# Kernel optimization log

Measured on AMD Instinct MI355X. Metric: run time of the kernel, lower is better.

## Reference

```python
import jax, jax.numpy as jnp
import numpy as np

HIDDEN = 3072
INTER = 8192
B, S = 4, 2048


def setup_inputs() -> dict:
    key = jax.random.key(0)
    k1, k2, k3, k4, k5 = jax.random.split(key, 5)
    hidden_states = jax.random.normal(k1, (B, S, HIDDEN), dtype=jnp.float32)
    # int8-valued quantized weights (stored as int32), per-output-channel scales
    gate_up_w_q = jax.random.randint(k2, (2 * INTER, HIDDEN), -128, 128, dtype=jnp.int32)
    gate_up_scale = jax.random.uniform(k3, (2 * INTER,), dtype=jnp.float32) * 0.01
    down_w_q = jax.random.randint(k4, (HIDDEN, INTER), -128, 128, dtype=jnp.int32)
    down_scale = jax.random.uniform(k5, (HIDDEN,), dtype=jnp.float32) * 0.01
    return {
        "hidden_states": hidden_states,
        "gate_up_w_q": gate_up_w_q,
        "gate_up_scale": gate_up_scale,
        "down_w_q": down_w_q,
        "down_scale": down_scale,
    }


def reference(hidden_states, gate_up_w_q, gate_up_scale, down_w_q, down_scale):
    # Inline dequant: W = W_q * scale (per output channel)
    w_gu = gate_up_w_q.astype(jnp.float32) * gate_up_scale[:, None]   # [2I, H]
    up_states = jnp.einsum("bsh,oh->bso", hidden_states, w_gu)        # [B, S, 2I]
    gate, up = jnp.split(up_states, 2, axis=-1)                       # each [B, S, I]
    h = up * jax.nn.silu(gate)                                        # SwiGLU
    w_d = down_w_q.astype(jnp.float32) * down_scale[:, None]          # [H, I]
    return jnp.einsum("bsi,hi->bsh", h, w_d)                          # [B, S, H]
```

## Files before the change

kernel.cpp:

```cpp
#include <hip/hip_runtime.h>
#include <hip/hip_bf16.h>

#define HIDDEN 3072
#define INTER  8192
#define NTOK   8192

typedef __attribute__((ext_vector_type(8))) short bf16x8;
typedef __attribute__((ext_vector_type(4))) float f32x4;

__device__ __forceinline__ void gload_lds16(const void* g, void* l) {
  __builtin_amdgcn_global_load_lds(
      (const __attribute__((address_space(1))) void*)g,
      (__attribute__((address_space(3))) void*)l, 16, 0, 0);
}

__device__ __forceinline__ unsigned short f2bf(float f) {
  unsigned int u = __builtin_bit_cast(unsigned int, f);
  u += 0x7fffu + ((u >> 16) & 1u);
  return (unsigned short)(u >> 16);
}


__global__ void cvt_f32_bf16(const float* __restrict__ in,
                             unsigned short* __restrict__ out, int n4) {
  int i = blockIdx.x * blockDim.x + threadIdx.x;
  if (i >= n4) return;
  float4 v = reinterpret_cast<const float4*>(in)[i];
  ushort4 o;
  o.x = f2bf(v.x); o.y = f2bf(v.y); o.z = f2bf(v.z); o.w = f2bf(v.w);
  reinterpret_cast<ushort4*>(out)[i] = o;
}

__global__ void cvt_i32_bf16(const int* __restrict__ in,
                             unsigned short* __restrict__ out, int n4) {
  int i = blockIdx.x * blockDim.x + threadIdx.x;
  if (i >= n4) return;
  int4 v = reinterpret_cast<const int4*>(in)[i];
  ushort4 o;
  o.x = f2bf((float)v.x); o.y = f2bf((float)v.y);
  o.z = f2bf((float)v.z); o.w = f2bf((float)v.w);
  reinterpret_cast<ushort4*>(out)[i] = o;
}

__global__ void cvt_wgu_perm(const int* __restrict__ in,
                             unsigned short* __restrict__ out) {
  int i4 = blockIdx.x * blockDim.x + threadIdx.x;
  const int RW = HIDDEN / 4;
  if (i4 >= 2 * INTER * RW) return;
  int rowp = i4 / RW;
  int col4 = i4 - rowp * RW;
  int c = ((rowp >> 5) << 4) + (rowp & 15);
  int u = (rowp >> 4) & 1;
  int srow = u * INTER + c;
  int4 v = reinterpret_cast<const int4*>(in)[(size_t)srow * RW + col4];
  ushort4 o;
  o.x = f2bf((float)v.x); o.y = f2bf((float)v.y);
  o.z = f2bf((float)v.z); o.w = f2bf((float)v.w);
  reinterpret_cast<ushort4*>(out)[i4] = o;
}


template<int K, int N>
__global__ __launch_bounds__(512, 2) void gemm8p(
    const unsigned short* __restrict__ A,
    const unsigned short* __restrict__ B,
    const float* __restrict__ scale,
    unsigned short* __restrict__ H)
{
  constexpr int NT = K / 64;
  __shared__ __align__(16) unsigned short lds[2][2][2][256 * 32];

  const int nbn = N / 256;
  const int nwg = (NTOK / 256) * nbn;
  int bid = blockIdx.x;
  int wg = (bid & 7) * (nwg >> 3) + (bid >> 3);
  const int bm = (wg / nbn) * 256;
  const int bn = (wg % nbn) * 256;

  const int tid  = threadIdx.x;
  const int lane = tid & 63;
  const int wid  = tid >> 6;
  const int wr = wid >> 2;
  const int wc = wid & 3;

  const int srow0 = tid >> 2;
  const int srow1 = 128 + (tid >> 2);
  const int scb   = tid & 3;

  const unsigned short* Ab = A + (size_t)bm * K;
  const unsigned short* Bb = B + (size_t)bn * K;

  auto stage = [&](const unsigned short* Gb, int op, int tt, int kh) {
    if (tt >= NT) return;
    int p = tt & 1;
    int kc = tt * 64 + kh * 32;
    unsigned short* lbase = &lds[p][op][kh][0];
    gload_lds16(Gb + (size_t)srow0 * K + kc + ((scb ^ ((srow0 >> 1) & 3)) * 8),
                lbase + (size_t)tid * 8);
    gload_lds16(Gb + (size_t)srow1 * K + kc + ((scb ^ ((srow1 >> 1) & 3)) * 8),
                lbase + (size_t)(512 + tid) * 8);
  };

  auto readA = [&](int p, int kh, int m) -> bf16x8 {
    int row = wr * 128 + m * 16 + (lane & 15);
    int cb = (lane >> 4) ^ ((row >> 1) & 3);
    return *(const bf16x8*)&lds[p][0][kh][row * 32 + cb * 8];
  };
  auto readB = [&](int p, int kh, int n) -> bf16x8 {
    int row = wc * 64 + n * 16 + (lane & 15);
    int cb = (lane >> 4) ^ ((row >> 1) & 3);
    return *(const bf16x8*)&lds[p][1][kh][row * 32 + cb * 8];
  };

  f32x4 acc[8][4] = {};
  bf16x8 aP[4], aQ[4], bP[4], bQ[4];

  stage(Ab, 0, 0, 0);
  stage(Bb, 1, 0, 0);
  stage(Ab, 0, 0, 1);
  stage(Bb, 1, 0, 1);
  asm volatile("s_waitcnt vmcnt(4)" ::: "memory");
  __builtin_amdgcn_s_barrier();
#pragma unroll
  for (int m = 0; m < 4; ++m) aP[m] = readA(0, 0, m);
#pragma unroll
  for (int n = 0; n < 4; ++n) bP[n] = readB(0, 0, n);

  for (int t = 0; t < NT; ++t) {
    const int pr = t & 1;

#pragma unroll
    for (int m = 0; m < 4; ++m) aQ[m] = readA(pr, 0, m + 4);
    stage(Ab, 0, t + 1, 0);
    __builtin_amdgcn_s_setprio(1);
#pragma unroll
    for (int m = 0; m < 4; ++m)
#pragma unroll
      for (int n = 0; n < 4; ++n)
        acc[m][n] = __builtin_amdgcn_mfma_f32_16x16x32_bf16(aP[m], bP[n], acc[m][n], 0, 0, 0);
    __builtin_amdgcn_s_setprio(0);

    if (t + 1 < NT) {
      asm volatile("s_waitcnt vmcnt(2)" ::: "memory");
    } else {
      asm volatile("s_waitcnt vmcnt(0)" ::: "memory");
    }
    __builtin_amdgcn_s_barrier();
#pragma unroll
    for (int m = 0; m < 4; ++m) aP[m] = readA(pr, 1, m);
#pragma unroll
    for (int n = 0; n < 4; ++n) bQ[n] = readB(pr, 1, n);
    stage(Bb, 1, t + 1, 0);
    __builtin_amdgcn_s_setprio(1);
#pragma unroll
    for (int m = 0; m < 4; ++m)
#pragma unroll
      for (int n = 0; n < 4; ++n)
        acc[m + 4][n] = __builtin_amdgcn_mfma_f32_16x16x32_bf16(aQ[m], bP[n], acc[m + 4][n], 0, 0, 0);
    __builtin_amdgcn_s_setprio(0);

#pragma unroll
    for (int m = 0; m < 4; ++m) aQ[m] = readA(pr, 1, m + 4);
    stage(Ab, 0, t + 1, 1);
    __builtin_amdgcn_s_setprio(1);
#pragma unroll
    for (int m = 0; m < 4; ++m)
#pragma unroll
      for (int n = 0; n < 4; ++n)
        acc[m][n] = __builtin_amdgcn_mfma_f32_16x16x32_bf16(aP[m], bQ[n], acc[m][n], 0, 0, 0);
    __builtin_amdgcn_s_setprio(0);

    asm volatile("s_waitcnt vmcnt(2)" ::: "memory");
    __builtin_amdgcn_s_barrier();
    if (t + 1 < NT) {
#pragma unroll
      for (int m = 0; m < 4; ++m) aP[m] = readA(pr ^ 1, 0, m);
#pragma unroll
      for (int n = 0; n < 4; ++n) bP[n] = readB(pr ^ 1, 0, n);
    }
    stage(Bb, 1, t + 1, 1);
    __builtin_amdgcn_s_setprio(1);
#pragma unroll
    for (int m = 0; m < 4; ++m)
#pragma unroll
      for (int n = 0; n < 4; ++n)
        acc[m + 4][n] = __builtin_amdgcn_mfma_f32_16x16x32_bf16(aQ[m], bQ[n], acc[m + 4][n], 0, 0, 0);
    __builtin_amdgcn_s_setprio(0);
  }

  const int crow0 = (lane >> 4) * 4;
  const int ccol  = lane & 15;
  const int hbase = (bn >> 1) + wc * 32;
#pragma unroll
  for (int np = 0; np < 2; ++np) {
    int hcol = hbase + np * 16 + ccol;
    float sg = scale[hcol];
    float su = scale[INTER + hcol];
#pragma unroll
    for (int m = 0; m < 8; ++m) {
#pragma unroll
      for (int j = 0; j < 4; ++j) {
        int row = bm + wr * 128 + m * 16 + crow0 + j;
        float g = acc[m][2 * np + 0][j] * sg;
        float u = acc[m][2 * np + 1][j] * su;
        float s = g / (1.0f + __expf(-g));
        H[(size_t)row * INTER + hcol] = f2bf(u * s);
      }
    }
  }
}


__global__ __launch_bounds__(512, 2) void gemm2k(
    const unsigned short* __restrict__ A,
    const unsigned short* __restrict__ B,
    const float* __restrict__ scale,
    float* __restrict__ O)
{
  constexpr int K = INTER;
  constexpr int NT = K / 64;
  __shared__ __align__(16) unsigned short ldsA[2][2][128 * 32];
  __shared__ __align__(16) unsigned short ldsB[2][2][256 * 32];

  const int nbn = HIDDEN / 256;
  const int nwg = (NTOK / 128) * nbn;
  int bid = blockIdx.x;
  int wg = (bid & 7) * (nwg >> 3) + (bid >> 3);
  const int bm = (wg / nbn) * 128;
  const int bn = (wg % nbn) * 256;

  const int tid  = threadIdx.x;
  const int lane = tid & 63;
  const int wid  = tid >> 6;
  const int wr = wid >> 2;
  const int wc = wid & 3;

  const int srow0 = tid >> 2;
  const int srow1 = 128 + (tid >> 2);
  const int scb   = tid & 3;

  const unsigned short* Ab = A + (size_t)bm * K;
  const unsigned short* Bb = B + (size_t)bn * K;

  auto stageA = [&](int tt, int kh) {
    if (tt >= NT) return;
    int p = tt & 1;
    int kc = tt * 64 + kh * 32;
    gload_lds16(Ab + (size_t)srow0 * K + kc + ((scb ^ ((srow0 >> 1) & 3)) * 8),
                &ldsA[p][kh][0] + (size_t)tid * 8);
  };
  auto stageB = [&](int tt, int kh) {
    if (tt >= NT) return;
    int p = tt & 1;
    int kc = tt * 64 + kh * 32;
    unsigned short* lbase = &ldsB[p][kh][0];
    gload_lds16(Bb + (size_t)srow0 * K + kc + ((scb ^ ((srow0 >> 1) & 3)) * 8),
                lbase + (size_t)tid * 8);
    gload_lds16(Bb + (size_t)srow1 * K + kc + ((scb ^ ((srow1 >> 1) & 3)) * 8),
                lbase + (size_t)(512 + tid) * 8);
  };

  auto readA = [&](int p, int kh, int m) -> bf16x8 {
    int row = wr * 64 + m * 16 + (lane & 15);
    int cb = (lane >> 4) ^ ((row >> 1) & 3);
    return *(const bf16x8*)&ldsA[p][kh][row * 32 + cb * 8];
  };
  auto readB = [&](int p, int kh, int n) -> bf16x8 {
    int row = wc * 64 + n * 16 + (lane & 15);
    int cb = (lane >> 4) ^ ((row >> 1) & 3);
    return *(const bf16x8*)&ldsB[p][kh][row * 32 + cb * 8];
  };

  f32x4 acc[4][4] = {};
  bf16x8 aF[4], bF[4];

  stageA(0, 0);
  stageB(0, 0);
  stageA(0, 1);
  stageB(0, 1);
  asm volatile("s_waitcnt vmcnt(3)" ::: "memory");
  __builtin_amdgcn_s_barrier();

  for (int t = 0; t < NT; ++t) {
    const int pr = t & 1;

#pragma unroll
    for (int m = 0; m < 4; ++m) aF[m] = readA(pr, 0, m);
#pragma unroll
    for (int n = 0; n < 4; ++n) bF[n] = readB(pr, 0, n);
    stageA(t + 1, 0);
    __builtin_amdgcn_s_setprio(1);
#pragma unroll
    for (int m = 0; m < 4; ++m)
#pragma unroll
      for (int n = 0; n < 4; ++n)
        acc[m][n] = __builtin_amdgcn_mfma_f32_16x16x32_bf16(aF[m], bF[n], acc[m][n], 0, 0, 0);
    __builtin_amdgcn_s_setprio(0);

    stageB(t + 1, 0);
    if (t + 1 < NT) {
      asm volatile("s_waitcnt vmcnt(3)" ::: "memory");
    } else {
      asm volatile("s_waitcnt vmcnt(0)" ::: "memory");
    }
    __builtin_amdgcn_s_barrier();

#pragma unroll
    for (int m = 0; m < 4; ++m) aF[m] = readA(pr, 1, m);
#pragma unroll
    for (int n = 0; n < 4; ++n) bF[n] = readB(pr, 1, n);
    stageA(t + 1, 1);
    __builtin_amdgcn_s_setprio(1);
#pragma unroll
    for (int m = 0; m < 4; ++m)
#pragma unroll
      for (int n = 0; n < 4; ++n)
        acc[m][n] = __builtin_amdgcn_mfma_f32_16x16x32_bf16(aF[m], bF[n], acc[m][n], 0, 0, 0);
    __builtin_amdgcn_s_setprio(0);

    stageB(t + 1, 1);
    asm volatile("s_waitcnt vmcnt(3)" ::: "memory");
    __builtin_amdgcn_s_barrier();
  }

  const int crow0 = (lane >> 4) * 4;
  const int ccol  = lane & 15;
#pragma unroll
  for (int n = 0; n < 4; ++n) {
    int col = bn + wc * 64 + n * 16 + ccol;
    float sc = scale[col];
#pragma unroll
    for (int m = 0; m < 4; ++m) {
#pragma unroll
      for (int j = 0; j < 4; ++j) {
        int row = bm + wr * 64 + m * 16 + crow0 + j;
        O[(size_t)row * HIDDEN + col] = acc[m][n][j] * sc;
      }
    }
  }
}


extern "C" void kernel_launch(void* const* d_in, const int* in_sizes, int n_in,
                              void* d_out, int out_size, void* d_ws, size_t ws_size,
                              hipStream_t stream) {
  (void)in_sizes; (void)n_in; (void)out_size; (void)ws_size;

  const float* hidden = (const float*)d_in[0];
  const int*   guq    = (const int*)d_in[1];
  const float* gus    = (const float*)d_in[2];
  const int*   dwq    = (const int*)d_in[3];
  const float* dsc    = (const float*)d_in[4];
  float* out = (float*)d_out;

  char* ws = (char*)d_ws;
  unsigned short* xb  = (unsigned short*)(ws);
  unsigned short* wgu = (unsigned short*)(ws + 50331648ull);
  unsigned short* wd  = (unsigned short*)(ws + 150994944ull);
  unsigned short* hb  = (unsigned short*)(ws + 201326592ull);

  {
    int n4 = NTOK * HIDDEN / 4;
    cvt_f32_bf16<<<(n4 + 255) / 256, 256, 0, stream>>>(hidden, xb, n4);
  }
  {
    int n4 = 2 * INTER * HIDDEN / 4;
    cvt_wgu_perm<<<(n4 + 255) / 256, 256, 0, stream>>>(guq, wgu);
  }
  {
    int n4 = HIDDEN * INTER / 4;
    cvt_i32_bf16<<<(n4 + 255) / 256, 256, 0, stream>>>(dwq, wd, n4);
  }

  gemm8p<HIDDEN, 2 * INTER>
      <<<(NTOK / 256) * (2 * INTER / 256), 512, 0, stream>>>(xb, wgu, gus, hb);
  gemm2k<<<(NTOK / 128) * (HIDDEN / 256), 512, 0, stream>>>(hb, wd, dsc, out);
}
```

Before: 1.332 ms.

## Retile down-projection GEMM to 256x192 with ping-pong register pipelining

Replaces the 128x256 down-projection GEMM with a 256x192 tile kernel that uses a shared LDS buffer and prefetches A/B fragments one half-step ahead, interleaving staging with MFMA groups. The grid shrinks from 768 to 512 workgroups, which matches two workgroups per CU in a single wave and aims to remove the partial tail wave while raising arithmetic intensity per tile. The B staging still loads 256 rows per tile although only 192 are used, which adds redundant global traffic and reads past the weight buffer on the last column tile. It also adds an unused fp32-output mode to the gate/up kernel template.

Measured after the change: 1.242 ms (median of 2 runs). -6.8%, faster.

```diff
diff --git a/kernel.cpp b/kernel.cpp
--- a/kernel.cpp
+++ b/kernel.cpp
@@ -60,12 +60,12 @@
 }
 
 
-template<int K, int N>
+template<int K, int N, int MODE>
 __global__ __launch_bounds__(512, 2) void gemm8p(
     const unsigned short* __restrict__ A,
     const unsigned short* __restrict__ B,
     const float* __restrict__ scale,
-    unsigned short* __restrict__ H)
+    void* __restrict__ outv)
 {
   constexpr int NT = K / 64;
   __shared__ __align__(16) unsigned short lds[2][2][2][256 * 32];
@@ -190,28 +190,46 @@
 
   const int crow0 = (lane >> 4) * 4;
   const int ccol  = lane & 15;
-  const int hbase = (bn >> 1) + wc * 32;
-#pragma unroll
-  for (int np = 0; np < 2; ++np) {
-    int hcol = hbase + np * 16 + ccol;
-    float sg = scale[hcol];
-    float su = scale[INTER + hcol];
-#pragma unroll
-    for (int m = 0; m < 8; ++m) {
-#pragma unroll
-      for (int j = 0; j < 4; ++j) {
-        int row = bm + wr * 128 + m * 16 + crow0 + j;
-        float g = acc[m][2 * np + 0][j] * sg;
-        float u = acc[m][2 * np + 1][j] * su;
-        float s = g / (1.0f + __expf(-g));
-        H[(size_t)row * INTER + hcol] = f2bf(u * s);
+  if constexpr (MODE == 1) {
+    unsigned short* H = (unsigned short*)outv;
+    const int hbase = (bn >> 1) + wc * 32;
+#pragma unroll
+    for (int np = 0; np < 2; ++np) {
+      int hcol = hbase + np * 16 + ccol;
+      float sg = scale[hcol];
+      float su = scale[INTER + hcol];
+#pragma unroll
+      for (int m = 0; m < 8; ++m) {
+#pragma unroll
+        for (int j = 0; j < 4; ++j) {
+          int row = bm + wr * 128 + m * 16 + crow0 + j;
+          float g = acc[m][2 * np + 0][j] * sg;
+          float u = acc[m][2 * np + 1][j] * su;
+          float s = g / (1.0f + __expf(-g));
+          H[(size_t)row * INTER + hcol] = f2bf(u * s);
+        }
       }
     }
-  }
-}
-
-
-__global__ __launch_bounds__(512, 2) void gemm2k(
+  } else {
+    float* O = (float*)outv;
+#pragma unroll
+    for (int n = 0; n < 4; ++n) {
+      int col = bn + wc * 64 + n * 16 + ccol;
+      float sc = scale[col];
+#pragma unroll
+      for (int m = 0; m < 8; ++m) {
+#pragma unroll
+        for (int j = 0; j < 4; ++j) {
+          int row = bm + wr * 128 + m * 16 + crow0 + j;
+          O[(size_t)row * N + col] = acc[m][n][j] * sc;
+        }
+      }
+    }
+  }
+}
+
+
+__global__ __launch_bounds__(512, 2) void gemm2_192(
     const unsigned short* __restrict__ A,
     const unsigned short* __restrict__ B,
     const float* __restrict__ scale,
@@ -219,15 +237,14 @@
 {
   constexpr int K = INTER;
   constexpr int NT = K / 64;
-  __shared__ __align__(16) unsigned short ldsA[2][2][128 * 32];
-  __shared__ __align__(16) unsigned short ldsB[2][2][256 * 32];
-
-  const int nbn = HIDDEN / 256;
-  const int nwg = (NTOK / 128) * nbn;
+  __shared__ __align__(16) unsigned short lds[2][2][2][256 * 32];
+
+  const int nbn = HIDDEN / 192;
+  const int nwg = (NTOK / 256) * nbn;
   int bid = blockIdx.x;
   int wg = (bid & 7) * (nwg >> 3) + (bid >> 3);
-  const int bm = (wg / nbn) * 128;
-  const int bn = (wg % nbn) * 256;
+  const int bm = (wg / nbn) * 256;
+  const int bn = (wg % nbn) * 192;
 
   const int tid  = threadIdx.x;
   const int lane = tid & 63;
@@ -242,98 +259,115 @@
   const unsigned short* Ab = A + (size_t)bm * K;
   const unsigned short* Bb = B + (size_t)bn * K;
 
-  auto stageA = [&](int tt, int kh) {
+  auto stage = [&](const unsigned short* Gb, int op, int tt, int kh) {
     if (tt >= NT) return;
     int p = tt & 1;
     int kc = tt * 64 + kh * 32;
-    gload_lds16(Ab + (size_t)srow0 * K + kc + ((scb ^ ((srow0 >> 1) & 3)) * 8),
-                &ldsA[p][kh][0] + (size_t)tid * 8);
-  };
-  auto stageB = [&](int tt, int kh) {
-    if (tt >= NT) return;
-    int p = tt & 1;
-    int kc = tt * 64 + kh * 32;
-    unsigned short* lbase = &ldsB[p][kh][0];
-    gload_lds16(Bb + (size_t)srow0 * K + kc + ((scb ^ ((srow0 >> 1) & 3)) * 8),
+    unsigned short* lbase = &lds[p][op][kh][0];
+    gload_lds16(Gb + (size_t)srow0 * K + kc + ((scb ^ ((srow0 >> 1) & 3)) * 8),
                 lbase + (size_t)tid * 8);
-    gload_lds16(Bb + (size_t)srow1 * K + kc + ((scb ^ ((srow1 >> 1) & 3)) * 8),
+    gload_lds16(Gb + (size_t)srow1 * K + kc + ((scb ^ ((srow1 >> 1) & 3)) * 8),
                 lbase + (size_t)(512 + tid) * 8);
   };
 
   auto readA = [&](int p, int kh, int m) -> bf16x8 {
-    int row = wr * 64 + m * 16 + (lane & 15);
+    int row = wr * 128 + m * 16 + (lane & 15);
     int cb = (lane >> 4) ^ ((row >> 1) & 3);
-    return *(const bf16x8*)&ldsA[p][kh][row * 32 + cb * 8];
+    return *(const bf16x8*)&lds[p][0][kh][row * 32 + cb * 8];
   };
   auto readB = [&](int p, int kh, int n) -> bf16x8 {
-    int row = wc * 64 + n * 16 + (lane & 15);
+    int row = wc * 48 + n * 16 + (lane & 15);
     int cb = (lane >> 4) ^ ((row >> 1) & 3);
-    return *(const bf16x8*)&ldsB[p][kh][row * 32 + cb * 8];
-  };
-
-  f32x4 acc[4][4] = {};
-  bf16x8 aF[4], bF[4];
-
-  stageA(0, 0);
-  stageB(0, 0);
-  stageA(0, 1);
-  stageB(0, 1);
-  asm volatile("s_waitcnt vmcnt(3)" ::: "memory");
+    return *(const bf16x8*)&lds[p][1][kh][row * 32 + cb * 8];
+  };
+
+  f32x4 acc[8][3] = {};
+  bf16x8 aP[4], aQ[4], bP[3], bQ[3];
+
+  stage(Ab, 0, 0, 0);
+  stage(Bb, 1, 0, 0);
+  stage(Ab, 0, 0, 1);
+  stage(Bb, 1, 0, 1);
+  asm volatile("s_waitcnt vmcnt(4)" ::: "memory");
   __builtin_amdgcn_s_barrier();
+#pragma unroll
+  for (int m = 0; m < 4; ++m) aP[m] = readA(0, 0, m);
+#pragma unroll
+  for (int n = 0; n < 3; ++n) bP[n] = readB(0, 0, n);
 
   for (int t = 0; t < NT; ++t) {
     const int pr = t & 1;
 
 #pragma unroll
-    for (int m = 0; m < 4; ++m) aF[m] = readA(pr, 0, m);
-#pragma unroll
-    for (int n = 0; n < 4; ++n) bF[n] = readB(pr, 0, n);
-    stageA(t + 1, 0);
-    __builtin_amdgcn_s_setprio(1);
-#pragma unroll
-    for (int m = 0; m < 4; ++m)
-#pragma unroll
-      for (int n = 0; n < 4; ++n)
-        acc[m][n] = __builtin_amdgcn_mfma_f32_16x16x32_bf16(aF[m], bF[n], acc[m][n], 0, 0, 0);
-    __builtin_amdgcn_s_setprio(0);
-
-    stageB(t + 1, 0);
+    for (int m = 0; m < 4; ++m) aQ[m] = readA(pr, 0, m + 4);
+    stage(Ab, 0, t + 1, 0);
+    __builtin_amdgcn_s_setprio(1);
+#pragma unroll
+    for (int m = 0; m < 4; ++m)
+#pragma unroll
+      for (int n = 0; n < 3; ++n)
+        acc[m][n] = __builtin_amdgcn_mfma_f32_16x16x32_bf16(aP[m], bP[n], acc[m][n], 0, 0, 0);
+    __builtin_amdgcn_s_setprio(0);
+
     if (t + 1 < NT) {
-      asm volatile("s_waitcnt vmcnt(3)" ::: "memory");
+      asm volatile("s_waitcnt vmcnt(2)" ::: "memory");
     } else {
       asm volatile("s_waitcnt vmcnt(0)" ::: "memory");
     }
     __builtin_amdgcn_s_barrier();
-
-#pragma unroll
-    for (int m = 0; m < 4; ++m) aF[m] = readA(pr, 1, m);
-#pragma unroll
-    for (int n = 0; n < 4; ++n) bF[n] = readB(pr, 1, n);
-    stageA(t + 1, 1);
-    __builtin_amdgcn_s_setprio(1);
-#pragma unroll
-    for (int m = 0; m < 4; ++m)
-#pragma unroll
-      for (int n = 0; n < 4; ++n)
-        acc[m][n] = __builtin_amdgcn_mfma_f32_16x16x32_bf16(aF[m], bF[n], acc[m][n], 0, 0, 0);
-    __builtin_amdgcn_s_setprio(0);
-
-    stageB(t + 1, 1);
-    asm volatile("s_waitcnt vmcnt(3)" ::: "memory");
+#pragma unroll
+    for (int m = 0; m < 4; ++m) aP[m] = readA(pr, 1, m);
+#pragma unroll
+    for (int n = 0; n < 3; ++n) bQ[n] = readB(pr, 1, n);
+    stage(Bb, 1, t + 1, 0);
+    __builtin_amdgcn_s_setprio(1);
+#pragma unroll
+    for (int m = 0; m < 4; ++m)
+#pragma unroll
+      for (int n = 0; n < 3; ++n)
+        acc[m + 4][n] = __builtin_amdgcn_mfma_f32_16x16x32_bf16(aQ[m], bP[n], acc[m + 4][n], 0, 0, 0);
+    __builtin_amdgcn_s_setprio(0);
+
+#pragma unroll
+    for (int m = 0; m < 4; ++m) aQ[m] = readA(pr, 1, m + 4);
+    stage(Ab, 0, t + 1, 1);
+    __builtin_amdgcn_s_setprio(1);
+#pragma unroll
+    for (int m = 0; m < 4; ++m)
+#pragma unroll
+      for (int n = 0; n < 3; ++n)
+        acc[m][n] = __builtin_amdgcn_mfma_f32_16x16x32_bf16(aP[m], bQ[n], acc[m][n], 0, 0, 0);
+    __builtin_amdgcn_s_setprio(0);
+
+    asm volatile("s_waitcnt vmcnt(2)" ::: "memory");
     __builtin_amdgcn_s_barrier();
+    if (t + 1 < NT) {
+#pragma unroll
+      for (int m = 0; m < 4; ++m) aP[m] = readA(pr ^ 1, 0, m);
+#pragma unroll
+      for (int n = 0; n < 3; ++n) bP[n] = readB(pr ^ 1, 0, n);
+    }
+    stage(Bb, 1, t + 1, 1);
+    __builtin_amdgcn_s_setprio(1);
+#pragma unroll
+    for (int m = 0; m < 4; ++m)
+#pragma unroll
+      for (int n = 0; n < 3; ++n)
+        acc[m + 4][n] = __builtin_amdgcn_mfma_f32_16x16x32_bf16(aQ[m], bQ[n], acc[m + 4][n], 0, 0, 0);
+    __builtin_amdgcn_s_setprio(0);
   }
 
   const int crow0 = (lane >> 4) * 4;
   const int ccol  = lane & 15;
 #pragma unroll
-  for (int n = 0; n < 4; ++n) {
-    int col = bn + wc * 64 + n * 16 + ccol;
+  for (int n = 0; n < 3; ++n) {
+    int col = bn + wc * 48 + n * 16 + ccol;
     float sc = scale[col];
 #pragma unroll
-    for (int m = 0; m < 4; ++m) {
+    for (int m = 0; m < 8; ++m) {
 #pragma unroll
       for (int j = 0; j < 4; ++j) {
-        int row = bm + wr * 64 + m * 16 + crow0 + j;
+        int row = bm + wr * 128 + m * 16 + crow0 + j;
         O[(size_t)row * HIDDEN + col] = acc[m][n][j] * sc;
       }
     }
@@ -372,7 +406,7 @@
     cvt_i32_bf16<<<(n4 + 255) / 256, 256, 0, stream>>>(dwq, wd, n4);
   }
 
-  gemm8p<HIDDEN, 2 * INTER>
+  gemm8p<HIDDEN, 2 * INTER, 1>
       <<<(NTOK / 256) * (2 * INTER / 256), 512, 0, stream>>>(xb, wgu, gus, hb);
-  gemm2k<<<(NTOK / 128) * (HIDDEN / 256), 512, 0, stream>>>(hb, wd, dsc, out);
-}
+  gemm2_192<<<(NTOK / 256) * (HIDDEN / 192), 512, 0, stream>>>(hb, wd, dsc, out);
+}
```
